# Kernel tuning notes

Hardware: AMD Instinct MI355X
Metric: run time of the kernel (lower is better)

Reference implementation:

```python
import jax, jax.numpy as jnp
import numpy as np

B, T, C, H = 2, 64, 384, 768
LR, MOM, DECAY = 0.01, 0.9, 0.001


def pscan(gates, tokens):
    """parallel_scan_log: x[t] = gates[t]*x[t-1] + tokens[t] along axis 1.
    gates [B,S], tokens [B,S,...]."""
    extra = tokens.ndim - gates.ndim
    g = gates.reshape(gates.shape + (1,) * extra)
    g = jnp.clip(g, 1e-7, 1.0 - 1e-7)
    lc = jnp.cumsum(jnp.log(g), axis=1)              # log cumulative gates
    return jnp.exp(lc) * jnp.cumsum(tokens * jnp.exp(-lc), axis=1)


def setup_inputs():
    key = jax.random.key(0)
    ks = jax.random.split(key, 12)
    s = 0.02
    W0 = jax.random.normal(ks[0], (H, C), jnp.float32) * s
    W1 = jax.random.normal(ks[1], (C, H), jnp.float32) * s
    return {
        "x": jax.random.normal(ks[2], (B, T, C), jnp.float32),
        "Wq": jax.random.normal(ks[3], (C, C), jnp.float32) * s, "bq": jnp.zeros((C,), jnp.float32),
        "Wk": jax.random.normal(ks[4], (C, C), jnp.float32) * s, "bk": jnp.zeros((C,), jnp.float32),
        "Wv": jax.random.normal(ks[5], (C, C), jnp.float32) * s, "bv": jnp.zeros((C,), jnp.float32),
        "Wo": jax.random.normal(ks[6], (C, C), jnp.float32) * s, "bo": jnp.zeros((C,), jnp.float32),
        "init_query": jax.random.normal(ks[7], (1, 1, C), jnp.float32) * s,
        "sW0": jnp.broadcast_to(W0, (B, H, C)) + 0.0,
        "sb0": jnp.zeros((B, H), jnp.float32),
        "sW1": jnp.broadcast_to(W1, (B, C, H)) + 0.0,
        "sb1": jnp.zeros((B, C), jnp.float32),
    }


def reference(x, Wq, bq, Wk, bk, Wv, bv, Wo, bo, init_query, sW0, sb0, sW1, sb1):
    dt = x.dtype
    # ---- retrieval (causal: uses init_query since no previous segment) ----
    q = jnp.broadcast_to(init_query, (B, 1, C)) @ Wq.T + bq          # [B,1,C]
    h_pre = jnp.einsum('bqc,bhc->bqh', q, sW0) + sb0[:, None]
    h = h_pre * jax.nn.sigmoid(h_pre)                                 # SiLU
    pred = jnp.einsum('bqh,bch->bqc', h, sW1) + sb1[:, None]
    out = pred @ Wo.T + bo                                            # [B,1,C]

    # ---- test-time memory update: per-token MSE gradients ----
    k = x @ Wk.T + bk                                                 # [B,T,C]
    v = x @ Wv.T + bv
    h1_pre = jnp.einsum('btc,bhc->bth', k, sW0) + sb0[:, None]
    sig = jax.nn.sigmoid(h1_pre)
    h1 = h1_pre * sig
    p = jnp.einsum('bth,bch->btc', h1, sW1) + sb1[:, None]
    dp = p - v                                                        # d(MSE)/d(pred)
    dW1 = jnp.einsum('btc,bth->btch', dp, h1)                         # [B,T,C,H]
    db1 = dp
    dh1 = jnp.einsum('btc,bch->bth', dp, sW1)
    dh1p = dh1 * (sig * (1 + h1_pre * (1 - sig)))                     # SiLU grad
    dW0 = jnp.einsum('bth,btc->bthc', dh1p, k)                        # [B,T,H,C]
    db0 = dh1p

    # ---- momentum scan + decayed weight scan ----
    def update(W, g):
        surprise = -LR * g                                            # [B,T,...]
        m = pscan(jnp.full((B, T), MOM, dt), (1.0 - MOM) * surprise)  # EMA of surprises
        toks = jnp.concatenate([W[:, None], m], axis=1)               # seed with current weight
        gts = jnp.concatenate([jnp.ones((B, 1), dt),
                               jnp.full((B, T), 1.0 - DECAY, dt)], axis=1)
        return pscan(gts, toks)[:, -1]                                # final weight after segment

    nW0 = update(sW0, dW0)
    nb0 = update(sb0, db0)
    nW1 = update(sW1, dW1)
    nb1 = update(sb1, db1)
    return out, nW0, nb0, nW1, nb1
```

## Files before the change

kernel.cpp:

```cpp
#include <hip/hip_runtime.h>
#include <hip/hip_bf16.h>
#include <cmath>

#define BB 2
#define TT 64
#define CC 384
#define HH 768

#define O_OUT 0
#define O_NW0 768
#define O_NB0 (768 + 589824)
#define O_NW1 (O_NB0 + 1536)
#define O_NB1 (O_NW1 + 589824)

struct Coefs { float ct[TT]; float dfac; };

typedef __attribute__((ext_vector_type(8))) short bf16x8;
typedef __attribute__((ext_vector_type(4))) float f32x4;

__device__ __forceinline__ float bf2f(unsigned short u) {
    union { unsigned int i; float f; } x; x.i = ((unsigned int)u) << 16; return x.f;
}
__device__ __forceinline__ unsigned short f2bf(float f) {
    union { float f; unsigned int i; } u; u.f = f;
    unsigned int x = u.i;
    unsigned int r = (x + 0x7fffu + ((x >> 16) & 1u)) >> 16;
    return (unsigned short)r;
}
__device__ __forceinline__ f32x4 mfma16(bf16x8 a, bf16x8 b, f32x4 c) {
    return __builtin_amdgcn_mfma_f32_16x16x32_bf16(a, b, c, 0, 0, 0);
}
__device__ __forceinline__ bf16x8 ldbf8(const unsigned short* p) {
    return *(const bf16x8*)p;
}

__global__ void k_conv(const float* __restrict__ x,  const float* __restrict__ Wq,
                       const float* __restrict__ Wk, const float* __restrict__ Wv,
                       const float* __restrict__ Wo, const float* __restrict__ sW0,
                       const float* __restrict__ sW1,
                       unsigned short* __restrict__ x_bf,  unsigned short* __restrict__ Wq_bf,
                       unsigned short* __restrict__ Wk_bf, unsigned short* __restrict__ Wv_bf,
                       unsigned short* __restrict__ Wo_bf, unsigned short* __restrict__ sW0_bf,
                       unsigned short* __restrict__ sW1_bf, unsigned short* __restrict__ sW1T_bf) {
    const int blk = blockIdx.x, j = threadIdx.x;
    if (blk < 1776) {
        int g = blk * 256 + j;
        const float* src; unsigned short* dst; int off;
        if      (g < 12288)  { src = x;   dst = x_bf;   off = g; }
        else if (g < 49152)  { src = Wq;  dst = Wq_bf;  off = g - 12288; }
        else if (g < 86016)  { src = Wk;  dst = Wk_bf;  off = g - 49152; }
        else if (g < 122880) { src = Wv;  dst = Wv_bf;  off = g - 86016; }
        else if (g < 159744) { src = Wo;  dst = Wo_bf;  off = g - 122880; }
        else if (g < 307200) { src = sW0; dst = sW0_bf; off = g - 159744; }
        else                 { src = sW1; dst = sW1_bf; off = g - 307200; }
        float4 v = ((const float4*)src)[off];
        ushort4 u;
        u.x = f2bf(v.x); u.y = f2bf(v.y); u.z = f2bf(v.z); u.w = f2bf(v.w);
        ((ushort4*)dst)[off] = u;
    } else {
        __shared__ float tile[32][33];
        const int r2 = blk - 1776;
        const int b = r2 / 288, rem = r2 % 288;
        const int c0 = (rem / 24) * 32, h0 = (rem % 24) * 32;
        const int row0 = j / 32, col = j % 32;
        #pragma unroll
        for (int r = 0; r < 4; ++r) {
            int row = row0 + r * 8;
            tile[row][col] = sW1[((size_t)(b * CC + c0 + row)) * HH + h0 + col];
        }
        __syncthreads();
        #pragma unroll
        for (int r = 0; r < 4; ++r) {
            int row = row0 + r * 8;
            sW1T_bf[((size_t)(b * HH + h0 + row)) * CC + c0 + col] = f2bf(tile[col][row]);
        }
    }
}

__global__ void k_qkv(const unsigned short* __restrict__ x_bf,
                      const unsigned short* __restrict__ Wk_bf, const float* __restrict__ bk,
                      const unsigned short* __restrict__ Wv_bf, const float* __restrict__ bv,
                      const unsigned short* __restrict__ Wq_bf, const float* __restrict__ bq,
                      const float* __restrict__ iq,
                      unsigned short* __restrict__ kb_bf, float* __restrict__ vb,
                      float* __restrict__ qb) {
    __shared__ float vecs[CC];
    __shared__ float part[16][17];
    const int blk = blockIdx.x, j = threadIdx.x;
    if (blk < 24) {
        const int wid = j >> 6, L = j & 63;
        const int w = blk * 4 + wid;
        const int mp = w % 4, np = w / 4;
        const int lrow = L & 15, kq = (L >> 4) * 8;
        const unsigned short* A0 = x_bf + (size_t)(mp * 32 + lrow) * CC;
        const unsigned short* A1 = A0 + 16 * CC;
        const int n0 = (2 * np) * 16 + lrow, n1 = n0 + 16;
        const unsigned short* B0 = (n0 < CC) ? (Wk_bf + (size_t)n0 * CC) : (Wv_bf + (size_t)(n0 - CC) * CC);
        const unsigned short* B1 = (n1 < CC) ? (Wk_bf + (size_t)n1 * CC) : (Wv_bf + (size_t)(n1 - CC) * CC);
        f32x4 acc00 = {0,0,0,0}, acc01 = {0,0,0,0}, acc10 = {0,0,0,0}, acc11 = {0,0,0,0};
        for (int s = 0; s < CC / 32; ++s) {
            int k = s * 32 + kq;
            bf16x8 a0 = ldbf8(A0 + k), a1 = ldbf8(A1 + k);
            bf16x8 b0 = ldbf8(B0 + k), b1 = ldbf8(B1 + k);
            acc00 = mfma16(a0, b0, acc00); acc01 = mfma16(a0, b1, acc01);
            acc10 = mfma16(a1, b0, acc10); acc11 = mfma16(a1, b1, acc11);
        }
        const int quad = L >> 4;
        #pragma unroll
        for (int mi = 0; mi < 2; ++mi) {
            #pragma unroll
            for (int ni = 0; ni < 2; ++ni) {
                f32x4 acc = mi == 0 ? (ni == 0 ? acc00 : acc01) : (ni == 0 ? acc10 : acc11);
                int n = (2 * np + ni) * 16 + lrow;
                #pragma unroll
                for (int r = 0; r < 4; ++r) {
                    int m = mp * 32 + mi * 16 + quad * 4 + r;
                    float v = acc[r];
                    if (n < CC) kb_bf[(size_t)m * CC + n] = f2bf(v + bk[n]);
                    else        vb[(size_t)m * CC + (n - CC)] = v + bv[n - CC];
                }
            }
        }
    } else {
        if (j < CC / 4) ((float4*)vecs)[j] = ((const float4*)iq)[j];
        __syncthreads();
        const int nt = blk - 24;
        const int nl = j & 15, ks = j >> 4;
        const int n = nt * 16 + nl;
        const unsigned short* wr = Wq_bf + (size_t)n * CC + ks * 24;
        float s = 0.f;
        for (int i = 0; i < 3; ++i) {
            bf16x8 wv8 = ldbf8(wr + i * 8);
            #pragma unroll
            for (int e = 0; e < 8; ++e)
                s += bf2f((unsigned short)wv8[e]) * vecs[ks * 24 + i * 8 + e];
        }
        part[ks][nl] = s;
        __syncthreads();
        if (j < 16) {
            float acc = bq[nt * 16 + j];
            #pragma unroll
            for (int kk = 0; kk < 16; ++kk) acc += part[kk][j];
            qb[nt * 16 + j] = acc;
        }
    }
}

__global__ void k_h1(const unsigned short* __restrict__ kb_bf, const float* __restrict__ qb,
                     const unsigned short* __restrict__ sW0_bf, const float* __restrict__ sb0,
                     unsigned short* __restrict__ h1_bf, float* __restrict__ dsil,
                     float* __restrict__ hret) {
    __shared__ float vecs[CC];
    __shared__ float part[16][17];
    const int blk = blockIdx.x, j = threadIdx.x;
    if (blk < 24) {
        const int b = blk / 12;
        const int wid = j >> 6, L = j & 63;
        const int w = (blk % 12) * 4 + wid;
        const int mp = w & 1, np = w >> 1;
        const int lrow = L & 15, kq = (L >> 4) * 8;
        const unsigned short* A0 = kb_bf + (size_t)(b * TT + mp * 32 + lrow) * CC;
        const unsigned short* A1 = A0 + 16 * CC;
        const int n0 = (2 * np) * 16 + lrow;
        const unsigned short* B0 = sW0_bf + (size_t)(b * HH + n0) * CC;
        const unsigned short* B1 = B0 + 16 * CC;
        f32x4 acc00 = {0,0,0,0}, acc01 = {0,0,0,0}, acc10 = {0,0,0,0}, acc11 = {0,0,0,0};
        for (int s = 0; s < CC / 32; ++s) {
            int k = s * 32 + kq;
            bf16x8 a0 = ldbf8(A0 + k), a1 = ldbf8(A1 + k);
            bf16x8 b0 = ldbf8(B0 + k), b1 = ldbf8(B1 + k);
            acc00 = mfma16(a0, b0, acc00); acc01 = mfma16(a0, b1, acc01);
            acc10 = mfma16(a1, b0, acc10); acc11 = mfma16(a1, b1, acc11);
        }
        const int quad = L >> 4;
        #pragma unroll
        for (int mi = 0; mi < 2; ++mi) {
            #pragma unroll
            for (int ni = 0; ni < 2; ++ni) {
                f32x4 acc = mi == 0 ? (ni == 0 ? acc00 : acc01) : (ni == 0 ? acc10 : acc11);
                int n = (2 * np + ni) * 16 + lrow;
                float bias = sb0[b * HH + n];
                #pragma unroll
                for (int r = 0; r < 4; ++r) {
                    int t = mp * 32 + mi * 16 + quad * 4 + r;
                    float pre = acc[r] + bias;
                    float sig = 1.f / (1.f + expf(-pre));
                    size_t idx = (size_t)(b * TT + t) * HH + n;
                    h1_bf[idx] = f2bf(pre * sig);
                    dsil[idx]  = sig * (1.f + pre * (1.f - sig));
                }
            }
        }
    } else {
        if (j < CC / 4) ((float4*)vecs)[j] = ((const float4*)qb)[j];
        __syncthreads();
        const int rb = blk - 24;
        const int b = rb / 48, nt = rb % 48;
        const int nl = j & 15, ks = j >> 4;
        const int n = nt * 16 + nl;
        const unsigned short* wr = sW0_bf + (size_t)(b * HH + n) * CC + ks * 24;
        float s = 0.f;
        for (int i = 0; i < 3; ++i) {
            bf16x8 wv8 = ldbf8(wr + i * 8);
            #pragma unroll
            for (int e = 0; e < 8; ++e)
                s += bf2f((unsigned short)wv8[e]) * vecs[ks * 24 + i * 8 + e];
        }
        part[ks][nl] = s;
        __syncthreads();
        if (j < 16) {
            int n2 = nt * 16 + j;
            float pre = sb0[b * HH + n2];
            #pragma unroll
            for (int kk = 0; kk < 16; ++kk) pre += part[kk][j];
            float sig = 1.f / (1.f + expf(-pre));
            hret[b * HH + n2] = pre * sig;
        }
    }
}

__global__ void k_p(const unsigned short* __restrict__ h1_bf, const float* __restrict__ hret,
                    const float* __restrict__ vb,
                    const unsigned short* __restrict__ sW1_bf, const float* __restrict__ sb1,
                    unsigned short* __restrict__ dp_bf, float* __restrict__ pred) {
    __shared__ float vecs[HH];
    __shared__ float part[16][17];
    const int blk = blockIdx.x, j = threadIdx.x;
    if (blk < 12) {
        const int b = blk / 6;
        const int wid = j >> 6, L = j & 63;
        const int w = (blk % 6) * 4 + wid;
        const int mp = w & 1, np = w >> 1;
        const int lrow = L & 15, kq = (L >> 4) * 8;
        const unsigned short* A0 = h1_bf + (size_t)(b * TT + mp * 32 + lrow) * HH;
        const unsigned short* A1 = A0 + 16 * HH;
        const int n0 = (2 * np) * 16 + lrow;
        const unsigned short* B0 = sW1_bf + (size_t)(b * CC + n0) * HH;
        const unsigned short* B1 = B0 + 16 * HH;
        f32x4 acc00 = {0,0,0,0}, acc01 = {0,0,0,0}, acc10 = {0,0,0,0}, acc11 = {0,0,0,0};
        for (int s = 0; s < HH / 32; ++s) {
            int k = s * 32 + kq;
            bf16x8 a0 = ldbf8(A0 + k), a1 = ldbf8(A1 + k);
            bf16x8 b0 = ldbf8(B0 + k), b1 = ldbf8(B1 + k);
            acc00 = mfma16(a0, b0, acc00); acc01 = mfma16(a0, b1, acc01);
            acc10 = mfma16(a1, b0, acc10); acc11 = mfma16(a1, b1, acc11);
        }
        const int quad = L >> 4;
        #pragma unroll
        for (int mi = 0; mi < 2; ++mi) {
            #pragma unroll
            for (int ni = 0; ni < 2; ++ni) {
                f32x4 acc = mi == 0 ? (ni == 0 ? acc00 : acc01) : (ni == 0 ? acc10 : acc11);
                int n = (2 * np + ni) * 16 + lrow;
                float bias = sb1[b * CC + n];
                #pragma unroll
                for (int r = 0; r < 4; ++r) {
                    int t = mp * 32 + mi * 16 + quad * 4 + r;
                    size_t idx = (size_t)(b * TT + t) * CC + n;
                    dp_bf[idx] = f2bf(acc[r] + bias - vb[idx]);
                }
            }
        }
    } else {
        const int rb = blk - 12;
        const int b = rb / 24, nt = rb % 24;
        if (j < HH / 4) ((float4*)vecs)[j] = ((const float4*)(hret + b * HH))[j];
        __syncthreads();
        const int nl = j & 15, ks = j >> 4;
        const int n = nt * 16 + nl;
        const unsigned short* wr = sW1_bf + (size_t)(b * CC + n) * HH + ks * 48;
        float s = 0.f;
        for (int i = 0; i < 6; ++i) {
            bf16x8 wv8 = ldbf8(wr + i * 8);
            #pragma unroll
            for (int e = 0; e < 8; ++e)
                s += bf2f((unsigned short)wv8[e]) * vecs[ks * 48 + i * 8 + e];
        }
        part[ks][nl] = s;
        __syncthreads();
        if (j < 16) {
            int n2 = nt * 16 + j;
            float acc = sb1[b * CC + n2];
            #pragma unroll
            for (int kk = 0; kk < 16; ++kk) acc += part[kk][j];
            pred[b * CC + n2] = acc;
        }
    }
}

__global__ void k_dh1(const unsigned short* __restrict__ dp_bf,
                      const unsigned short* __restrict__ sW1T_bf,
                      const float* __restrict__ dsil,
                      unsigned short* __restrict__ dh1p_bf) {
    const int blk = blockIdx.x, j = threadIdx.x;
    const int b = blk / 12;
    const int wid = j >> 6, L = j & 63;
    const int w = (blk % 12) * 4 + wid;
    const int mp = w & 1, np = w >> 1;
    const int lrow = L & 15, kq = (L >> 4) * 8;
    const unsigned short* A0 = dp_bf + (size_t)(b * TT + mp * 32 + lrow) * CC;
    const unsigned short* A1 = A0 + 16 * CC;
    const int n0 = (2 * np) * 16 + lrow;
    const unsigned short* B0 = sW1T_bf + (size_t)(b * HH + n0) * CC;
    const unsigned short* B1 = B0 + 16 * CC;
    f32x4 acc00 = {0,0,0,0}, acc01 = {0,0,0,0}, acc10 = {0,0,0,0}, acc11 = {0,0,0,0};
    for (int s = 0; s < CC / 32; ++s) {
        int k = s * 32 + kq;
        bf16x8 a0 = ldbf8(A0 + k), a1 = ldbf8(A1 + k);
        bf16x8 b0 = ldbf8(B0 + k), b1 = ldbf8(B1 + k);
        acc00 = mfma16(a0, b0, acc00); acc01 = mfma16(a0, b1, acc01);
        acc10 = mfma16(a1, b0, acc10); acc11 = mfma16(a1, b1, acc11);
    }
    const int quad = L >> 4;
    #pragma unroll
    for (int mi = 0; mi < 2; ++mi) {
        #pragma unroll
        for (int ni = 0; ni < 2; ++ni) {
            f32x4 acc = mi == 0 ? (ni == 0 ? acc00 : acc01) : (ni == 0 ? acc10 : acc11);
            int n = (2 * np + ni) * 16 + lrow;
            #pragma unroll
            for (int r = 0; r < 4; ++r) {
                int t = mp * 32 + mi * 16 + quad * 4 + r;
                size_t idx = (size_t)(b * TT + t) * HH + n;
                dh1p_bf[idx] = f2bf(acc[r] * dsil[idx]);
            }
        }
    }
}

__global__ void k_epi(const unsigned short* __restrict__ dp_bf,
                      const unsigned short* __restrict__ h1_bf,
                      const unsigned short* __restrict__ dh1p_bf,
                      const unsigned short* __restrict__ kb_bf,
                      const float* __restrict__ pred,
                      const float* __restrict__ sW0, const float* __restrict__ sb0,
                      const float* __restrict__ sW1, const float* __restrict__ sb1,
                      const unsigned short* __restrict__ Wo_bf, const float* __restrict__ bo,
                      float* __restrict__ out, Coefs cf) {
    __shared__ float a_t[TT][32];
    __shared__ float e_t[TT][64];
    __shared__ float vecs[CC];
    __shared__ float part[16][17];
    const int blk = blockIdx.x, j = threadIdx.x;

    if (blk < 288) {
        const int b = blk / 144, rem = blk % 144;
        const int c0 = (rem / 12) * 32, h0 = (rem % 12) * 64;
        for (int i = j; i < TT * 32; i += 256) {
            int t = i >> 5, c = i & 31;
            a_t[t][c] = cf.ct[t] * bf2f(dp_bf[((size_t)(b * TT + t)) * CC + c0 + c]);
        }
        for (int i = j; i < TT * 64; i += 256) {
            int t = i >> 6, h = i & 63;
            e_t[t][h] = bf2f(h1_bf[((size_t)(b * TT + t)) * HH + h0 + h]);
        }
        __syncthreads();
        const int ci = j & 31, hb = (j >> 5) * 8;
        float acc[8] = {0, 0, 0, 0, 0, 0, 0, 0};
        for (int t = 0; t < TT; ++t) {
            float av = a_t[t][ci];
            #pragma unroll
            for (int m = 0; m < 8; ++m) acc[m] += av * e_t[t][hb + m];
        }
        const size_t idx = ((size_t)b * CC + c0 + ci) * HH + h0 + hb;
        const float4* w4 = (const float4*)(sW1 + idx);
        float4 wa = w4[0], wb = w4[1];
        float4 o0, o1;
        o0.x = cf.dfac * wa.x - acc[0]; o0.y = cf.dfac * wa.y - acc[1];
        o0.z = cf.dfac * wa.z - acc[2]; o0.w = cf.dfac * wa.w - acc[3];
        o1.x = cf.dfac * wb.x - acc[4]; o1.y = cf.dfac * wb.y - acc[5];
        o1.z = cf.dfac * wb.z - acc[6]; o1.w = cf.dfac * wb.w - acc[7];
        *(float4*)(out + O_NW1 + idx) = o0;
        *(float4*)(out + O_NW1 + idx + 4) = o1;
    } else if (blk < 576) {
        const int bk2 = blk - 288;
        const int b = bk2 / 144, rem = bk2 % 144;
        const int h0 = (rem / 6) * 32, c0 = (rem % 6) * 64;
        for (int i = j; i < TT * 32; i += 256) {
            int t = i >> 5, h = i & 31;
            a_t[t][h] = cf.ct[t] * bf2f(dh1p_bf[((size_t)(b * TT + t)) * HH + h0 + h]);
        }
        for (int i = j; i < TT * 64; i += 256) {
            int t = i >> 6, c = i & 63;
            e_t[t][c] = bf2f(kb_bf[((size_t)(b * TT + t)) * CC + c0 + c]);
        }
        __syncthreads();
        const int hi = j & 31, cb = (j >> 5) * 8;
        float acc[8] = {0, 0, 0, 0, 0, 0, 0, 0};
        for (int t = 0; t < TT; ++t) {
            float av = a_t[t][hi];
            #pragma unroll
            for (int m = 0; m < 8; ++m) acc[m] += av * e_t[t][cb + m];
        }
        const size_t idx = ((size_t)b * HH + h0 + hi) * CC + c0 + cb;
        const float4* w4 = (const float4*)(sW0 + idx);
        float4 wa = w4[0], wb = w4[1];
        float4 o0, o1;
        o0.x = cf.dfac * wa.x - acc[0]; o0.y = cf.dfac * wa.y - acc[1];
        o0.z = cf.dfac * wa.z - acc[2]; o0.w = cf.dfac * wa.w - acc[3];
        o1.x = cf.dfac * wb.x - acc[4]; o1.y = cf.dfac * wb.y - acc[5];
        o1.z = cf.dfac * wb.z - acc[6]; o1.w = cf.dfac * wb.w - acc[7];
        *(float4*)(out + O_NW0 + idx) = o0;
        *(float4*)(out + O_NW0 + idx + 4) = o1;
    } else if (blk < 624) {
        const int rb = blk - 576;
        const int b = rb / 24, nt = rb % 24;
        if (j < CC / 4) ((float4*)vecs)[j] = ((const float4*)(pred + b * CC))[j];
        __syncthreads();
        const int nl = j & 15, ks = j >> 4;
        const int n = nt * 16 + nl;
        const unsigned short* wr = Wo_bf + (size_t)n * CC + ks * 24;
        float s = 0.f;
        for (int i = 0; i < 3; ++i) {
            bf16x8 wv8 = ldbf8(wr + i * 8);
            #pragma unroll
            for (int e = 0; e < 8; ++e)
                s += bf2f((unsigned short)wv8[e]) * vecs[ks * 24 + i * 8 + e];
        }
        part[ks][nl] = s;
        __syncthreads();
        if (j < 16) {
            int n2 = nt * 16 + j;
            float acc = bo[n2];
            #pragma unroll
            for (int kk = 0; kk < 16; ++kk) acc += part[kk][j];
            out[O_OUT + b * CC + n2] = acc;
        }
    } else {
        const int b = blk - 624;
        for (int c = j; c < CC; c += 256) {
            float acc = 0.f;
            for (int t = 0; t < TT; ++t)
                acc += cf.ct[t] * bf2f(dp_bf[((size_t)(b * TT + t)) * CC + c]);
            out[O_NB1 + b * CC + c] = cf.dfac * sb1[b * CC + c] - acc;
        }
        for (int h = j; h < HH; h += 256) {
            float acc = 0.f;
            for (int t = 0; t < TT; ++t)
                acc += cf.ct[t] * bf2f(dh1p_bf[((size_t)(b * TT + t)) * HH + h]);
            out[O_NB0 + b * HH + h] = cf.dfac * sb0[b * HH + h] - acc;
        }
    }
}

extern "C" void kernel_launch(void* const* d_in, const int* in_sizes, int n_in,
                              void* d_out, int out_size, void* d_ws, size_t ws_size,
                              hipStream_t stream) {
    const float* x   = (const float*)d_in[0];
    const float* Wq  = (const float*)d_in[1];
    const float* bq  = (const float*)d_in[2];
    const float* Wk  = (const float*)d_in[3];
    const float* bk  = (const float*)d_in[4];
    const float* Wv  = (const float*)d_in[5];
    const float* bv  = (const float*)d_in[6];
    const float* Wo  = (const float*)d_in[7];
    const float* bo  = (const float*)d_in[8];
    const float* iq  = (const float*)d_in[9];
    const float* sW0 = (const float*)d_in[10];
    const float* sb0 = (const float*)d_in[11];
    const float* sW1 = (const float*)d_in[12];
    const float* sb1 = (const float*)d_in[13];

    float* fw = (float*)d_ws;
    float* qb   = fw;
    float* hret = qb + 384;
    float* pred = hret + 1536;
    float* vb   = pred + 768;
    float* dsil = vb + 49152;
    unsigned short* us = (unsigned short*)(dsil + 98304);
    unsigned short* x_bf    = us;
    unsigned short* kb_bf   = x_bf + 49152;
    unsigned short* h1_bf   = kb_bf + 49152;
    unsigned short* dp_bf   = h1_bf + 98304;
    unsigned short* dh1p_bf = dp_bf + 49152;
    unsigned short* Wq_bf   = dh1p_bf + 98304;
    unsigned short* Wk_bf   = Wq_bf + 147456;
    unsigned short* Wv_bf   = Wk_bf + 147456;
    unsigned short* Wo_bf   = Wv_bf + 147456;
    unsigned short* sW0_bf  = Wo_bf + 147456;
    unsigned short* sW1_bf  = sW0_bf + 589824;
    unsigned short* sW1T_bf = sW1_bf + 589824;

    Coefs cf;
    const double mom = 0.9, decay = 1.0 - 0.001, lr = 0.01;
    for (int s = 0; s < TT; ++s) {
        double sum = 0.0;
        for (int t = s; t < TT; ++t) sum += pow(decay, (double)(TT - 1 - t)) * pow(mom, (double)(t - s));
        cf.ct[s] = (float)(lr * (1.0 - mom) * sum);
    }
    cf.dfac = (float)pow(decay, (double)TT);

    k_conv<<<dim3(1776 + 576), dim3(256), 0, stream>>>(x, Wq, Wk, Wv, Wo, sW0, sW1,
        x_bf, Wq_bf, Wk_bf, Wv_bf, Wo_bf, sW0_bf, sW1_bf, sW1T_bf);
    k_qkv<<<dim3(48), dim3(256), 0, stream>>>(x_bf, Wk_bf, bk, Wv_bf, bv, Wq_bf, bq, iq,
                                              kb_bf, vb, qb);
    k_h1 <<<dim3(120), dim3(256), 0, stream>>>(kb_bf, qb, sW0_bf, sb0, h1_bf, dsil, hret);
    k_p  <<<dim3(60), dim3(256), 0, stream>>>(h1_bf, hret, vb, sW1_bf, sb1, dp_bf, pred);
    k_dh1<<<dim3(24), dim3(256), 0, stream>>>(dp_bf, sW1T_bf, dsil, dh1p_bf);
    k_epi<<<dim3(626), dim3(256), 0, stream>>>(dp_bf, h1_bf, dh1p_bf, kb_bf, pred,
                                               sW0, sb0, sW1, sb1, Wo_bf, bo,
                                               (float*)d_out, cf);
}
```

Measured before the change: 144.6 us.

## Fuse six launches into one cooperative kernel with grid-wide syncs

Replaces the six separate kernel launches with one persistent cooperative kernel of 512 blocks whose stages are separated by grid.sync(). It also drops the bf16 conversions of Wq and Wo; the matrix-vector paths now read fp32 weights directly. The sW1 transpose pass writes both the plain and transposed bf16 copies from one shared tile. The aim is to remove per-launch overhead and gaps between launches, at the cost of grid barriers and many idle blocks in the small stages.

Measured after the change: 449.3 us. +210.6%, slower.

```diff
diff --git a/kernel.cpp b/kernel.cpp
--- a/kernel.cpp
+++ b/kernel.cpp
@@ -1,11 +1,15 @@
 #include <hip/hip_runtime.h>
 #include <hip/hip_bf16.h>
+#include <hip/hip_cooperative_groups.h>
 #include <cmath>
+
+namespace cg = cooperative_groups;
 
 #define BB 2
 #define TT 64
 #define CC 384
 #define HH 768
+#define GRID 512
 
 #define O_OUT 0
 #define O_NW0 768
@@ -18,6 +22,15 @@
 typedef __attribute__((ext_vector_type(8))) short bf16x8;
 typedef __attribute__((ext_vector_type(4))) float f32x4;
 
+struct Args {
+    const float *x, *Wq, *bq, *Wk, *bk, *Wv, *bv, *Wo, *bo, *iq, *sW0, *sb0, *sW1, *sb1;
+    unsigned short *x_bf, *Wk_bf, *Wv_bf, *sW0_bf, *sW1_bf, *sW1T_bf;
+    unsigned short *kb_bf, *h1_bf, *dp_bf, *dh1p_bf;
+    float *vb, *dsil, *qb, *hret, *pred;
+    float *out;
+    Coefs cf;
+};
+
 __device__ __forceinline__ float bf2f(unsigned short u) {
     union { unsigned int i; float f; } x; x.i = ((unsigned int)u) << 16; return x.f;
 }
@@ -34,69 +47,56 @@
     return *(const bf16x8*)p;
 }
 
-__global__ void k_conv(const float* __restrict__ x,  const float* __restrict__ Wq,
-                       const float* __restrict__ Wk, const float* __restrict__ Wv,
-                       const float* __restrict__ Wo, const float* __restrict__ sW0,
-                       const float* __restrict__ sW1,
-                       unsigned short* __restrict__ x_bf,  unsigned short* __restrict__ Wq_bf,
-                       unsigned short* __restrict__ Wk_bf, unsigned short* __restrict__ Wv_bf,
-                       unsigned short* __restrict__ Wo_bf, unsigned short* __restrict__ sW0_bf,
-                       unsigned short* __restrict__ sW1_bf, unsigned short* __restrict__ sW1T_bf) {
+__global__ void __launch_bounds__(256, 2) k_fused(Args A) {
+    __shared__ float smem[6144];
+    cg::grid_group grid = cg::this_grid();
     const int blk = blockIdx.x, j = threadIdx.x;
-    if (blk < 1776) {
-        int g = blk * 256 + j;
-        const float* src; unsigned short* dst; int off;
-        if      (g < 12288)  { src = x;   dst = x_bf;   off = g; }
-        else if (g < 49152)  { src = Wq;  dst = Wq_bf;  off = g - 12288; }
-        else if (g < 86016)  { src = Wk;  dst = Wk_bf;  off = g - 49152; }
-        else if (g < 122880) { src = Wv;  dst = Wv_bf;  off = g - 86016; }
-        else if (g < 159744) { src = Wo;  dst = Wo_bf;  off = g - 122880; }
-        else if (g < 307200) { src = sW0; dst = sW0_bf; off = g - 159744; }
-        else                 { src = sW1; dst = sW1_bf; off = g - 307200; }
-        float4 v = ((const float4*)src)[off];
-        ushort4 u;
-        u.x = f2bf(v.x); u.y = f2bf(v.y); u.z = f2bf(v.z); u.w = f2bf(v.w);
-        ((ushort4*)dst)[off] = u;
-    } else {
-        __shared__ float tile[32][33];
-        const int r2 = blk - 1776;
-        const int b = r2 / 288, rem = r2 % 288;
-        const int c0 = (rem / 24) * 32, h0 = (rem % 24) * 32;
-        const int row0 = j / 32, col = j % 32;
-        #pragma unroll
-        for (int r = 0; r < 4; ++r) {
-            int row = row0 + r * 8;
-            tile[row][col] = sW1[((size_t)(b * CC + c0 + row)) * HH + h0 + col];
-        }
-        __syncthreads();
-        #pragma unroll
-        for (int r = 0; r < 4; ++r) {
-            int row = row0 + r * 8;
-            sW1T_bf[((size_t)(b * HH + h0 + row)) * CC + c0 + col] = f2bf(tile[col][row]);
-        }
-    }
-}
-
-__global__ void k_qkv(const unsigned short* __restrict__ x_bf,
-                      const unsigned short* __restrict__ Wk_bf, const float* __restrict__ bk,
-                      const unsigned short* __restrict__ Wv_bf, const float* __restrict__ bv,
-                      const unsigned short* __restrict__ Wq_bf, const float* __restrict__ bq,
-                      const float* __restrict__ iq,
-                      unsigned short* __restrict__ kb_bf, float* __restrict__ vb,
-                      float* __restrict__ qb) {
-    __shared__ float vecs[CC];
-    __shared__ float part[16][17];
-    const int blk = blockIdx.x, j = threadIdx.x;
+    const Coefs& cf = A.cf;
+
+    {
+        int tid = blk * 256 + j;
+        for (int g = tid; g < 233472; g += GRID * 256) {
+            const float* src; unsigned short* dst; int off;
+            if      (g < 12288) { src = A.x;   dst = A.x_bf;   off = g; }
+            else if (g < 49152) { src = A.Wk;  dst = A.Wk_bf;  off = g - 12288; }
+            else if (g < 86016) { src = A.Wv;  dst = A.Wv_bf;  off = g - 49152; }
+            else                { src = A.sW0; dst = A.sW0_bf; off = g - 86016; }
+            float4 v = ((const float4*)src)[off];
+            ushort4 u;
+            u.x = f2bf(v.x); u.y = f2bf(v.y); u.z = f2bf(v.z); u.w = f2bf(v.w);
+            ((ushort4*)dst)[off] = u;
+        }
+        for (int u = blk; u < 576; u += GRID) {
+            const int b = u / 288, rem = u % 288;
+            const int c0 = (rem / 24) * 32, h0 = (rem % 24) * 32;
+            const int row0 = j >> 5, col = j & 31;
+            __syncthreads();
+            #pragma unroll
+            for (int r = 0; r < 4; ++r) {
+                int row = row0 + r * 8;
+                smem[row * 33 + col] = A.sW1[((size_t)(b * CC + c0 + row)) * HH + h0 + col];
+            }
+            __syncthreads();
+            #pragma unroll
+            for (int r = 0; r < 4; ++r) {
+                int row = row0 + r * 8;
+                A.sW1_bf [((size_t)(b * CC + c0 + row)) * HH + h0 + col] = f2bf(smem[row * 33 + col]);
+                A.sW1T_bf[((size_t)(b * HH + h0 + row)) * CC + c0 + col] = f2bf(smem[col * 33 + row]);
+            }
+        }
+    }
+    grid.sync();
+
     if (blk < 24) {
         const int wid = j >> 6, L = j & 63;
         const int w = blk * 4 + wid;
         const int mp = w % 4, np = w / 4;
         const int lrow = L & 15, kq = (L >> 4) * 8;
-        const unsigned short* A0 = x_bf + (size_t)(mp * 32 + lrow) * CC;
+        const unsigned short* A0 = A.x_bf + (size_t)(mp * 32 + lrow) * CC;
         const unsigned short* A1 = A0 + 16 * CC;
         const int n0 = (2 * np) * 16 + lrow, n1 = n0 + 16;
-        const unsigned short* B0 = (n0 < CC) ? (Wk_bf + (size_t)n0 * CC) : (Wv_bf + (size_t)(n0 - CC) * CC);
-        const unsigned short* B1 = (n1 < CC) ? (Wk_bf + (size_t)n1 * CC) : (Wv_bf + (size_t)(n1 - CC) * CC);
+        const unsigned short* B0 = (n0 < CC) ? (A.Wk_bf + (size_t)n0 * CC) : (A.Wv_bf + (size_t)(n0 - CC) * CC);
+        const unsigned short* B1 = (n1 < CC) ? (A.Wk_bf + (size_t)n1 * CC) : (A.Wv_bf + (size_t)(n1 - CC) * CC);
         f32x4 acc00 = {0,0,0,0}, acc01 = {0,0,0,0}, acc10 = {0,0,0,0}, acc11 = {0,0,0,0};
         for (int s = 0; s < CC / 32; ++s) {
             int k = s * 32 + kq;
@@ -116,53 +116,46 @@
                 for (int r = 0; r < 4; ++r) {
                     int m = mp * 32 + mi * 16 + quad * 4 + r;
                     float v = acc[r];
-                    if (n < CC) kb_bf[(size_t)m * CC + n] = f2bf(v + bk[n]);
-                    else        vb[(size_t)m * CC + (n - CC)] = v + bv[n - CC];
+                    if (n < CC) A.kb_bf[(size_t)m * CC + n] = f2bf(v + A.bk[n]);
+                    else        A.vb[(size_t)m * CC + (n - CC)] = v + A.bv[n - CC];
                 }
             }
         }
-    } else {
-        if (j < CC / 4) ((float4*)vecs)[j] = ((const float4*)iq)[j];
+    } else if (blk < 48) {
+        if (j < CC / 4) ((float4*)smem)[j] = ((const float4*)A.iq)[j];
         __syncthreads();
         const int nt = blk - 24;
         const int nl = j & 15, ks = j >> 4;
         const int n = nt * 16 + nl;
-        const unsigned short* wr = Wq_bf + (size_t)n * CC + ks * 24;
+        const float4* wr = (const float4*)(A.Wq + (size_t)n * CC + ks * 24);
         float s = 0.f;
-        for (int i = 0; i < 3; ++i) {
-            bf16x8 wv8 = ldbf8(wr + i * 8);
-            #pragma unroll
-            for (int e = 0; e < 8; ++e)
-                s += bf2f((unsigned short)wv8[e]) * vecs[ks * 24 + i * 8 + e];
-        }
-        part[ks][nl] = s;
+        #pragma unroll
+        for (int i = 0; i < 6; ++i) {
+            float4 a = wr[i];
+            const float* v = smem + ks * 24 + i * 4;
+            s += a.x * v[0] + a.y * v[1] + a.z * v[2] + a.w * v[3];
+        }
+        smem[1024 + ks * 17 + nl] = s;
         __syncthreads();
         if (j < 16) {
-            float acc = bq[nt * 16 + j];
-            #pragma unroll
-            for (int kk = 0; kk < 16; ++kk) acc += part[kk][j];
-            qb[nt * 16 + j] = acc;
-        }
-    }
-}
-
-__global__ void k_h1(const unsigned short* __restrict__ kb_bf, const float* __restrict__ qb,
-                     const unsigned short* __restrict__ sW0_bf, const float* __restrict__ sb0,
-                     unsigned short* __restrict__ h1_bf, float* __restrict__ dsil,
-                     float* __restrict__ hret) {
-    __shared__ float vecs[CC];
-    __shared__ float part[16][17];
-    const int blk = blockIdx.x, j = threadIdx.x;
+            float acc = A.bq[nt * 16 + j];
+            #pragma unroll
+            for (int kk = 0; kk < 16; ++kk) acc += smem[1024 + kk * 17 + j];
+            A.qb[nt * 16 + j] = acc;
+        }
+    }
+    grid.sync();
+
     if (blk < 24) {
         const int b = blk / 12;
         const int wid = j >> 6, L = j & 63;
         const int w = (blk % 12) * 4 + wid;
         const int mp = w & 1, np = w >> 1;
         const int lrow = L & 15, kq = (L >> 4) * 8;
-        const unsigned short* A0 = kb_bf + (size_t)(b * TT + mp * 32 + lrow) * CC;
+        const unsigned short* A0 = A.kb_bf + (size_t)(b * TT + mp * 32 + lrow) * CC;
         const unsigned short* A1 = A0 + 16 * CC;
         const int n0 = (2 * np) * 16 + lrow;
-        const unsigned short* B0 = sW0_bf + (size_t)(b * HH + n0) * CC;
+        const unsigned short* B0 = A.sW0_bf + (size_t)(b * HH + n0) * CC;
         const unsigned short* B1 = B0 + 16 * CC;
         f32x4 acc00 = {0,0,0,0}, acc01 = {0,0,0,0}, acc10 = {0,0,0,0}, acc11 = {0,0,0,0};
         for (int s = 0; s < CC / 32; ++s) {
@@ -179,63 +172,56 @@
             for (int ni = 0; ni < 2; ++ni) {
                 f32x4 acc = mi == 0 ? (ni == 0 ? acc00 : acc01) : (ni == 0 ? acc10 : acc11);
                 int n = (2 * np + ni) * 16 + lrow;
-                float bias = sb0[b * HH + n];
+                float bias = A.sb0[b * HH + n];
                 #pragma unroll
                 for (int r = 0; r < 4; ++r) {
                     int t = mp * 32 + mi * 16 + quad * 4 + r;
                     float pre = acc[r] + bias;
                     float sig = 1.f / (1.f + expf(-pre));
                     size_t idx = (size_t)(b * TT + t) * HH + n;
-                    h1_bf[idx] = f2bf(pre * sig);
-                    dsil[idx]  = sig * (1.f + pre * (1.f - sig));
+                    A.h1_bf[idx] = f2bf(pre * sig);
+                    A.dsil[idx]  = sig * (1.f + pre * (1.f - sig));
                 }
             }
         }
-    } else {
-        if (j < CC / 4) ((float4*)vecs)[j] = ((const float4*)qb)[j];
+    } else if (blk < 120) {
+        if (j < CC / 4) ((float4*)smem)[j] = ((const float4*)A.qb)[j];
         __syncthreads();
         const int rb = blk - 24;
         const int b = rb / 48, nt = rb % 48;
         const int nl = j & 15, ks = j >> 4;
         const int n = nt * 16 + nl;
-        const unsigned short* wr = sW0_bf + (size_t)(b * HH + n) * CC + ks * 24;
+        const float4* wr = (const float4*)(A.sW0 + (size_t)(b * HH + n) * CC + ks * 24);
         float s = 0.f;
-        for (int i = 0; i < 3; ++i) {
-            bf16x8 wv8 = ldbf8(wr + i * 8);
-            #pragma unroll
-            for (int e = 0; e < 8; ++e)
-                s += bf2f((unsigned short)wv8[e]) * vecs[ks * 24 + i * 8 + e];
-        }
-        part[ks][nl] = s;
+        #pragma unroll
+        for (int i = 0; i < 6; ++i) {
+            float4 a = wr[i];
+            const float* v = smem + ks * 24 + i * 4;
+            s += a.x * v[0] + a.y * v[1] + a.z * v[2] + a.w * v[3];
+        }
+        smem[1024 + ks * 17 + nl] = s;
         __syncthreads();
         if (j < 16) {
             int n2 = nt * 16 + j;
-            float pre = sb0[b * HH + n2];
-            #pragma unroll
-            for (int kk = 0; kk < 16; ++kk) pre += part[kk][j];
+            float pre = A.sb0[b * HH + n2];
+            #pragma unroll
+            for (int kk = 0; kk < 16; ++kk) pre += smem[1024 + kk * 17 + j];
             float sig = 1.f / (1.f + expf(-pre));
-            hret[b * HH + n2] = pre * sig;
-        }
-    }
-}
-
-__global__ void k_p(const unsigned short* __restrict__ h1_bf, const float* __restrict__ hret,
-                    const float* __restrict__ vb,
-                    const unsigned short* __restrict__ sW1_bf, const float* __restrict__ sb1,
-                    unsigned short* __restrict__ dp_bf, float* __restrict__ pred) {
-    __shared__ float vecs[HH];
-    __shared__ float part[16][17];
-    const int blk = blockIdx.x, j = threadIdx.x;
+            A.hret[b * HH + n2] = pre * sig;
+        }
+    }
+    grid.sync();
+
     if (blk < 12) {
         const int b = blk / 6;
         const int wid = j >> 6, L = j & 63;
         const int w = (blk % 6) * 4 + wid;
         const int mp = w & 1, np = w >> 1;
         const int lrow = L & 15, kq = (L >> 4) * 8;
-        const unsigned short* A0 = h1_bf + (size_t)(b * TT + mp * 32 + lrow) * HH;
+        const unsigned short* A0 = A.h1_bf + (size_t)(b * TT + mp * 32 + lrow) * HH;
         const unsigned short* A1 = A0 + 16 * HH;
         const int n0 = (2 * np) * 16 + lrow;
-        const unsigned short* B0 = sW1_bf + (size_t)(b * CC + n0) * HH;
+        const unsigned short* B0 = A.sW1_bf + (size_t)(b * CC + n0) * HH;
         const unsigned short* B1 = B0 + 16 * HH;
         f32x4 acc00 = {0,0,0,0}, acc01 = {0,0,0,0}, acc10 = {0,0,0,0}, acc11 = {0,0,0,0};
         for (int s = 0; s < HH / 32; ++s) {
@@ -252,193 +238,182 @@
             for (int ni = 0; ni < 2; ++ni) {
                 f32x4 acc = mi == 0 ? (ni == 0 ? acc00 : acc01) : (ni == 0 ? acc10 : acc11);
                 int n = (2 * np + ni) * 16 + lrow;
-                float bias = sb1[b * CC + n];
+                float bias = A.sb1[b * CC + n];
                 #pragma unroll
                 for (int r = 0; r < 4; ++r) {
                     int t = mp * 32 + mi * 16 + quad * 4 + r;
                     size_t idx = (size_t)(b * TT + t) * CC + n;
-                    dp_bf[idx] = f2bf(acc[r] + bias - vb[idx]);
+                    A.dp_bf[idx] = f2bf(acc[r] + bias - A.vb[idx]);
                 }
             }
         }
-    } else {
+    } else if (blk < 60) {
         const int rb = blk - 12;
         const int b = rb / 24, nt = rb % 24;
-        if (j < HH / 4) ((float4*)vecs)[j] = ((const float4*)(hret + b * HH))[j];
+        if (j < HH / 4) ((float4*)smem)[j] = ((const float4*)(A.hret + b * HH))[j];
         __syncthreads();
         const int nl = j & 15, ks = j >> 4;
         const int n = nt * 16 + nl;
-        const unsigned short* wr = sW1_bf + (size_t)(b * CC + n) * HH + ks * 48;
+        const float4* wr = (const float4*)(A.sW1 + (size_t)(b * CC + n) * HH + ks * 48);
         float s = 0.f;
-        for (int i = 0; i < 6; ++i) {
-            bf16x8 wv8 = ldbf8(wr + i * 8);
-            #pragma unroll
-            for (int e = 0; e < 8; ++e)
-                s += bf2f((unsigned short)wv8[e]) * vecs[ks * 48 + i * 8 + e];
-        }
-        part[ks][nl] = s;
+        #pragma unroll
+        for (int i = 0; i < 12; ++i) {
+            float4 a = wr[i];
+            const float* v = smem + ks * 48 + i * 4;
+            s += a.x * v[0] + a.y * v[1] + a.z * v[2] + a.w * v[3];
+        }
+        smem[1024 + ks * 17 + nl] = s;
         __syncthreads();
         if (j < 16) {
             int n2 = nt * 16 + j;
-            float acc = sb1[b * CC + n2];
-            #pragma unroll
-            for (int kk = 0; kk < 16; ++kk) acc += part[kk][j];
-            pred[b * CC + n2] = acc;
-        }
-    }
-}
-
-__global__ void k_dh1(const unsigned short* __restrict__ dp_bf,
-                      const unsigned short* __restrict__ sW1T_bf,
-                      const float* __restrict__ dsil,
-                      unsigned short* __restrict__ dh1p_bf) {
-    const int blk = blockIdx.x, j = threadIdx.x;
-    const int b = blk / 12;
-    const int wid = j >> 6, L = j & 63;
-    const int w = (blk % 12) * 4 + wid;
-    const int mp = w & 1, np = w >> 1;
-    const int lrow = L & 15, kq = (L >> 4) * 8;
-    const unsigned short* A0 = dp_bf + (size_t)(b * TT + mp * 32 + lrow) * CC;
-    const unsigned short* A1 = A0 + 16 * CC;
-    const int n0 = (2 * np) * 16 + lrow;
-    const unsigned short* B0 = sW1T_bf + (size_t)(b * HH + n0) * CC;
-    const unsigned short* B1 = B0 + 16 * CC;
-    f32x4 acc00 = {0,0,0,0}, acc01 = {0,0,0,0}, acc10 = {0,0,0,0}, acc11 = {0,0,0,0};
-    for (int s = 0; s < CC / 32; ++s) {
-        int k = s * 32 + kq;
-        bf16x8 a0 = ldbf8(A0 + k), a1 = ldbf8(A1 + k);
-        bf16x8 b0 = ldbf8(B0 + k), b1 = ldbf8(B1 + k);
-        acc00 = mfma16(a0, b0, acc00); acc01 = mfma16(a0, b1, acc01);
-        acc10 = mfma16(a1, b0, acc10); acc11 = mfma16(a1, b1, acc11);
-    }
-    const int quad = L >> 4;
-    #pragma unroll
-    for (int mi = 0; mi < 2; ++mi) {
-        #pragma unroll
-        for (int ni = 0; ni < 2; ++ni) {
-            f32x4 acc = mi == 0 ? (ni == 0 ? acc00 : acc01) : (ni == 0 ? acc10 : acc11);
-            int n = (2 * np + ni) * 16 + lrow;
-            #pragma unroll
-            for (int r = 0; r < 4; ++r) {
-                int t = mp * 32 + mi * 16 + quad * 4 + r;
-                size_t idx = (size_t)(b * TT + t) * HH + n;
-                dh1p_bf[idx] = f2bf(acc[r] * dsil[idx]);
-            }
-        }
-    }
-}
-
-__global__ void k_epi(const unsigned short* __restrict__ dp_bf,
-                      const unsigned short* __restrict__ h1_bf,
-                      const unsigned short* __restrict__ dh1p_bf,
-                      const unsigned short* __restrict__ kb_bf,
-                      const float* __restrict__ pred,
-                      const float* __restrict__ sW0, const float* __restrict__ sb0,
-                      const float* __restrict__ sW1, const float* __restrict__ sb1,
-                      const unsigned short* __restrict__ Wo_bf, const float* __restrict__ bo,
-                      float* __restrict__ out, Coefs cf) {
-    __shared__ float a_t[TT][32];
-    __shared__ float e_t[TT][64];
-    __shared__ float vecs[CC];
-    __shared__ float part[16][17];
-    const int blk = blockIdx.x, j = threadIdx.x;
-
-    if (blk < 288) {
-        const int b = blk / 144, rem = blk % 144;
-        const int c0 = (rem / 12) * 32, h0 = (rem % 12) * 64;
-        for (int i = j; i < TT * 32; i += 256) {
-            int t = i >> 5, c = i & 31;
-            a_t[t][c] = cf.ct[t] * bf2f(dp_bf[((size_t)(b * TT + t)) * CC + c0 + c]);
-        }
-        for (int i = j; i < TT * 64; i += 256) {
-            int t = i >> 6, h = i & 63;
-            e_t[t][h] = bf2f(h1_bf[((size_t)(b * TT + t)) * HH + h0 + h]);
-        }
-        __syncthreads();
-        const int ci = j & 31, hb = (j >> 5) * 8;
-        float acc[8] = {0, 0, 0, 0, 0, 0, 0, 0};
-        for (int t = 0; t < TT; ++t) {
-            float av = a_t[t][ci];
-            #pragma unroll
-            for (int m = 0; m < 8; ++m) acc[m] += av * e_t[t][hb + m];
-        }
-        const size_t idx = ((size_t)b * CC + c0 + ci) * HH + h0 + hb;
-        const float4* w4 = (const float4*)(sW1 + idx);
-        float4 wa = w4[0], wb = w4[1];
-        float4 o0, o1;
-        o0.x = cf.dfac * wa.x - acc[0]; o0.y = cf.dfac * wa.y - acc[1];
-        o0.z = cf.dfac * wa.z - acc[2]; o0.w = cf.dfac * wa.w - acc[3];
-        o1.x = cf.dfac * wb.x - acc[4]; o1.y = cf.dfac * wb.y - acc[5];
-        o1.z = cf.dfac * wb.z - acc[6]; o1.w = cf.dfac * wb.w - acc[7];
-        *(float4*)(out + O_NW1 + idx) = o0;
-        *(float4*)(out + O_NW1 + idx + 4) = o1;
-    } else if (blk < 576) {
-        const int bk2 = blk - 288;
-        const int b = bk2 / 144, rem = bk2 % 144;
-        const int h0 = (rem / 6) * 32, c0 = (rem % 6) * 64;
-        for (int i = j; i < TT * 32; i += 256) {
-            int t = i >> 5, h = i & 31;
-            a_t[t][h] = cf.ct[t] * bf2f(dh1p_bf[((size_t)(b * TT + t)) * HH + h0 + h]);
-        }
-        for (int i = j; i < TT * 64; i += 256) {
-            int t = i >> 6, c = i & 63;
-            e_t[t][c] = bf2f(kb_bf[((size_t)(b * TT + t)) * CC + c0 + c]);
-        }
-        __syncthreads();
-        const int hi = j & 31, cb = (j >> 5) * 8;
-        float acc[8] = {0, 0, 0, 0, 0, 0, 0, 0};
-        for (int t = 0; t < TT; ++t) {
-            float av = a_t[t][hi];
-            #pragma unroll
-            for (int m = 0; m < 8; ++m) acc[m] += av * e_t[t][cb + m];
-        }
-        const size_t idx = ((size_t)b * HH + h0 + hi) * CC + c0 + cb;
-        const float4* w4 = (const float4*)(sW0 + idx);
-        float4 wa = w4[0], wb = w4[1];
-        float4 o0, o1;
-        o0.x = cf.dfac * wa.x - acc[0]; o0.y = cf.dfac * wa.y - acc[1];
-        o0.z = cf.dfac * wa.z - acc[2]; o0.w = cf.dfac * wa.w - acc[3];
-        o1.x = cf.dfac * wb.x - acc[4]; o1.y = cf.dfac * wb.y - acc[5];
-        o1.z = cf.dfac * wb.z - acc[6]; o1.w = cf.dfac * wb.w - acc[7];
-        *(float4*)(out + O_NW0 + idx) = o0;
-        *(float4*)(out + O_NW0 + idx + 4) = o1;
-    } else if (blk < 624) {
-        const int rb = blk - 576;
-        const int b = rb / 24, nt = rb % 24;
-        if (j < CC / 4) ((float4*)vecs)[j] = ((const float4*)(pred + b * CC))[j];
-        __syncthreads();
-        const int nl = j & 15, ks = j >> 4;
-        const int n = nt * 16 + nl;
-        const unsigned short* wr = Wo_bf + (size_t)n * CC + ks * 24;
-        float s = 0.f;
-        for (int i = 0; i < 3; ++i) {
-            bf16x8 wv8 = ldbf8(wr + i * 8);
-            #pragma unroll
-            for (int e = 0; e < 8; ++e)
-                s += bf2f((unsigned short)wv8[e]) * vecs[ks * 24 + i * 8 + e];
-        }
-        part[ks][nl] = s;
-        __syncthreads();
-        if (j < 16) {
-            int n2 = nt * 16 + j;
-            float acc = bo[n2];
-            #pragma unroll
-            for (int kk = 0; kk < 16; ++kk) acc += part[kk][j];
-            out[O_OUT + b * CC + n2] = acc;
-        }
-    } else {
-        const int b = blk - 624;
-        for (int c = j; c < CC; c += 256) {
-            float acc = 0.f;
-            for (int t = 0; t < TT; ++t)
-                acc += cf.ct[t] * bf2f(dp_bf[((size_t)(b * TT + t)) * CC + c]);
-            out[O_NB1 + b * CC + c] = cf.dfac * sb1[b * CC + c] - acc;
-        }
-        for (int h = j; h < HH; h += 256) {
-            float acc = 0.f;
-            for (int t = 0; t < TT; ++t)
-                acc += cf.ct[t] * bf2f(dh1p_bf[((size_t)(b * TT + t)) * HH + h]);
-            out[O_NB0 + b * HH + h] = cf.dfac * sb0[b * HH + h] - acc;
+            float acc = A.sb1[b * CC + n2];
+            #pragma unroll
+            for (int kk = 0; kk < 16; ++kk) acc += smem[1024 + kk * 17 + j];
+            A.pred[b * CC + n2] = acc;
+        }
+    }
+    grid.sync();
+
+    if (blk < 24) {
+        const int b = blk / 12;
+        const int wid = j >> 6, L = j & 63;
+        const int w = (blk % 12) * 4 + wid;
+        const int mp = w & 1, np = w >> 1;
+        const int lrow = L & 15, kq = (L >> 4) * 8;
+        const unsigned short* A0 = A.dp_bf + (size_t)(b * TT + mp * 32 + lrow) * CC;
+        const unsigned short* A1 = A0 + 16 * CC;
+        const int n0 = (2 * np) * 16 + lrow;
+        const unsigned short* B0 = A.sW1T_bf + (size_t)(b * HH + n0) * CC;
+        const unsigned short* B1 = B0 + 16 * CC;
+        f32x4 acc00 = {0,0,0,0}, acc01 = {0,0,0,0}, acc10 = {0,0,0,0}, acc11 = {0,0,0,0};
+        for (int s = 0; s < CC / 32; ++s) {
+            int k = s * 32 + kq;
+            bf16x8 a0 = ldbf8(A0 + k), a1 = ldbf8(A1 + k);
+            bf16x8 b0 = ldbf8(B0 + k), b1 = ldbf8(B1 + k);
+            acc00 = mfma16(a0, b0, acc00); acc01 = mfma16(a0, b1, acc01);
+            acc10 = mfma16(a1, b0, acc10); acc11 = mfma16(a1, b1, acc11);
+        }
+        const int quad = L >> 4;
+        #pragma unroll
+        for (int mi = 0; mi < 2; ++mi) {
+            #pragma unroll
+            for (int ni = 0; ni < 2; ++ni) {
+                f32x4 acc = mi == 0 ? (ni == 0 ? acc00 : acc01) : (ni == 0 ? acc10 : acc11);
+                int n = (2 * np + ni) * 16 + lrow;
+                #pragma unroll
+                for (int r = 0; r < 4; ++r) {
+                    int t = mp * 32 + mi * 16 + quad * 4 + r;
+                    size_t idx = (size_t)(b * TT + t) * HH + n;
+                    A.dh1p_bf[idx] = f2bf(acc[r] * A.dsil[idx]);
+                }
+            }
+        }
+    }
+    grid.sync();
+
+    for (int u = blk; u < 626; u += GRID) {
+        __syncthreads();
+        if (u < 288) {
+            float* a_t = smem;
+            float* e_t = smem + 2048;
+            const int b = u / 144, rem = u % 144;
+            const int c0 = (rem / 12) * 32, h0 = (rem % 12) * 64;
+            for (int i = j; i < TT * 32; i += 256) {
+                int t = i >> 5, c = i & 31;
+                a_t[t * 32 + c] = cf.ct[t] * bf2f(A.dp_bf[((size_t)(b * TT + t)) * CC + c0 + c]);
+            }
+            for (int i = j; i < TT * 64; i += 256) {
+                int t = i >> 6, h = i & 63;
+                e_t[t * 64 + h] = bf2f(A.h1_bf[((size_t)(b * TT + t)) * HH + h0 + h]);
+            }
+            __syncthreads();
+            const int ci = j & 31, hb = (j >> 5) * 8;
+            float acc[8] = {0, 0, 0, 0, 0, 0, 0, 0};
+            for (int t = 0; t < TT; ++t) {
+                float av = a_t[t * 32 + ci];
+                #pragma unroll
+                for (int m = 0; m < 8; ++m) acc[m] += av * e_t[t * 64 + hb + m];
+            }
+            const size_t idx = ((size_t)b * CC + c0 + ci) * HH + h0 + hb;
+            const float4* w4 = (const float4*)(A.sW1 + idx);
+            float4 wa = w4[0], wb = w4[1];
+            float4 o0, o1;
+            o0.x = cf.dfac * wa.x - acc[0]; o0.y = cf.dfac * wa.y - acc[1];
+            o0.z = cf.dfac * wa.z - acc[2]; o0.w = cf.dfac * wa.w - acc[3];
+            o1.x = cf.dfac * wb.x - acc[4]; o1.y = cf.dfac * wb.y - acc[5];
+            o1.z = cf.dfac * wb.z - acc[6]; o1.w = cf.dfac * wb.w - acc[7];
+            *(float4*)(A.out + O_NW1 + idx) = o0;
+            *(float4*)(A.out + O_NW1 + idx + 4) = o1;
+        } else if (u < 576) {
+            float* a_t = smem;
+            float* e_t = smem + 2048;
+            const int u2 = u - 288;
+            const int b = u2 / 144, rem = u2 % 144;
+            const int h0 = (rem / 6) * 32, c0 = (rem % 6) * 64;
+            for (int i = j; i < TT * 32; i += 256) {
+                int t = i >> 5, h = i & 31;
+                a_t[t * 32 + h] = cf.ct[t] * bf2f(A.dh1p_bf[((size_t)(b * TT + t)) * HH + h0 + h]);
+            }
+            for (int i = j; i < TT * 64; i += 256) {
+                int t = i >> 6, c = i & 63;
+                e_t[t * 64 + c] = bf2f(A.kb_bf[((size_t)(b * TT + t)) * CC + c0 + c]);
+            }
+            __syncthreads();
+            const int hi = j & 31, cb = (j >> 5) * 8;
+            float acc[8] = {0, 0, 0, 0, 0, 0, 0, 0};
+            for (int t = 0; t < TT; ++t) {
+                float av = a_t[t * 32 + hi];
+                #pragma unroll
+                for (int m = 0; m < 8; ++m) acc[m] += av * e_t[t * 64 + cb + m];
+            }
+            const size_t idx = ((size_t)b * HH + h0 + hi) * CC + c0 + cb;
+            const float4* w4 = (const float4*)(A.sW0 + idx);
+            float4 wa = w4[0], wb = w4[1];
+            float4 o0, o1;
+            o0.x = cf.dfac * wa.x - acc[0]; o0.y = cf.dfac * wa.y - acc[1];
+            o0.z = cf.dfac * wa.z - acc[2]; o0.w = cf.dfac * wa.w - acc[3];
+            o1.x = cf.dfac * wb.x - acc[4]; o1.y = cf.dfac * wb.y - acc[5];
+            o1.z = cf.dfac * wb.z - acc[6]; o1.w = cf.dfac * wb.w - acc[7];
+            *(float4*)(A.out + O_NW0 + idx) = o0;
+            *(float4*)(A.out + O_NW0 + idx + 4) = o1;
+        } else if (u < 624) {
+            const int rb = u - 576;
+            const int b = rb / 24, nt = rb % 24;
+            if (j < CC / 4) ((float4*)smem)[j] = ((const float4*)(A.pred + b * CC))[j];
+            __syncthreads();
+            const int nl = j & 15, ks = j >> 4;
+            const int n = nt * 16 + nl;
+            const float4* wr = (const float4*)(A.Wo + (size_t)n * CC + ks * 24);
+            float s = 0.f;
+            #pragma unroll
+            for (int i = 0; i < 6; ++i) {
+                float4 a = wr[i];
+                const float* v = smem + ks * 24 + i * 4;
+                s += a.x * v[0] + a.y * v[1] + a.z * v[2] + a.w * v[3];
+            }
+            smem[1024 + ks * 17 + nl] = s;
+            __syncthreads();
+            if (j < 16) {
+                int n2 = nt * 16 + j;
+                float acc = A.bo[n2];
+                #pragma unroll
+                for (int kk = 0; kk < 16; ++kk) acc += smem[1024 + kk * 17 + j];
+                A.out[O_OUT + b * CC + n2] = acc;
+            }
+        } else {
+            const int b = u - 624;
+            for (int c = j; c < CC; c += 256) {
+                float acc = 0.f;
+                for (int t = 0; t < TT; ++t)
+                    acc += cf.ct[t] * bf2f(A.dp_bf[((size_t)(b * TT + t)) * CC + c]);
+                A.out[O_NB1 + b * CC + c] = cf.dfac * A.sb1[b * CC + c] - acc;
+            }
+            for (int h = j; h < HH; h += 256) {
+                float acc = 0.f;
+                for (int t = 0; t < TT; ++t)
+                    acc += cf.ct[t] * bf2f(A.dh1p_bf[((size_t)(b * TT + t)) * HH + h]);
+                A.out[O_NB0 + b * HH + h] = cf.dfac * A.sb0[b * HH + h] - acc;
+            }
         }
     }
 }
@@ -446,58 +421,49 @@
 extern "C" void kernel_launch(void* const* d_in, const int* in_sizes, int n_in,
                               void* d_out, int out_size, void* d_ws, size_t ws_size,
                               hipStream_t stream) {
-    const float* x   = (const float*)d_in[0];
-    const float* Wq  = (const float*)d_in[1];
-    const float* bq  = (const float*)d_in[2];
-    const float* Wk  = (const float*)d_in[3];
-    const float* bk  = (const float*)d_in[4];
-    const float* Wv  = (const float*)d_in[5];
-    const float* bv  = (const float*)d_in[6];
-    const float* Wo  = (const float*)d_in[7];
-    const float* bo  = (const float*)d_in[8];
-    const float* iq  = (const float*)d_in[9];
-    const float* sW0 = (const float*)d_in[10];
-    const float* sb0 = (const float*)d_in[11];
-    const float* sW1 = (const float*)d_in[12];
-    const float* sb1 = (const float*)d_in[13];
+    Args A;
+    A.x   = (const float*)d_in[0];
+    A.Wq  = (const float*)d_in[1];
+    A.bq  = (const float*)d_in[2];
+    A.Wk  = (const float*)d_in[3];
+    A.bk  = (const float*)d_in[4];
+    A.Wv  = (const float*)d_in[5];
+    A.bv  = (const float*)d_in[6];
+    A.Wo  = (const float*)d_in[7];
+    A.bo  = (const float*)d_in[8];
+    A.iq  = (const float*)d_in[9];
+    A.sW0 = (const float*)d_in[10];
+    A.sb0 = (const float*)d_in[11];
+    A.sW1 = (const float*)d_in[12];
+    A.sb1 = (const float*)d_in[13];
+    A.out = (float*)d_out;
 
     float* fw = (float*)d_ws;
-    float* qb   = fw;
-    float* hret = qb + 384;
-    float* pred = hret + 1536;
-    float* vb   = pred + 768;
-    float* dsil = vb + 49152;
-    unsigned short* us = (unsigned short*)(dsil + 98304);
-    unsigned short* x_bf    = us;
-    unsigned short* kb_bf   = x_bf + 49152;
-    unsigned short* h1_bf   = kb_bf + 49152;
-    unsigned short* dp_bf   = h1_bf + 98304;
-    unsigned short* dh1p_bf = dp_bf + 49152;
-    unsigned short* Wq_bf   = dh1p_bf + 98304;
-    unsigned short* Wk_bf   = Wq_bf + 147456;
-    unsigned short* Wv_bf   = Wk_bf + 147456;
-    unsigned short* Wo_bf   = Wv_bf + 147456;
-    unsigned short* sW0_bf  = Wo_bf + 147456;
-    unsigned short* sW1_bf  = sW0_bf + 589824;
-    unsigned short* sW1T_bf = sW1_bf + 589824;
-
-    Coefs cf;
+    A.qb   = fw;
+    A.hret = A.qb + 384;
+    A.pred = A.hret + 1536;
+    A.vb   = A.pred + 768;
+    A.dsil = A.vb + 49152;
+    unsigned short* us = (unsigned short*)(A.dsil + 98304);
+    A.x_bf    = us;
+    A.kb_bf   = A.x_bf + 49152;
+    A.h1_bf   = A.kb_bf + 49152;
+    A.dp_bf   = A.h1_bf + 98304;
+    A.dh1p_bf = A.dp_bf + 49152;
+    A.Wk_bf   = A.dh1p_bf + 98304;
+    A.Wv_bf   = A.Wk_bf + 147456;
+    A.sW0_bf  = A.Wv_bf + 147456;
+    A.sW1_bf  = A.sW0_bf + 589824;
+    A.sW1T_bf = A.sW1_bf + 589824;
+
     const double mom = 0.9, decay = 1.0 - 0.001, lr = 0.01;
     for (int s = 0; s < TT; ++s) {
         double sum = 0.0;
         for (int t = s; t < TT; ++t) sum += pow(decay, (double)(TT - 1 - t)) * pow(mom, (double)(t - s));
-        cf.ct[s] = (float)(lr * (1.0 - mom) * sum);
-    }
-    cf.dfac = (float)pow(decay, (double)TT);
-
-    k_conv<<<dim3(1776 + 576), dim3(256), 0, stream>>>(x, Wq, Wk, Wv, Wo, sW0, sW1,
-        x_bf, Wq_bf, Wk_bf, Wv_bf, Wo_bf, sW0_bf, sW1_bf, sW1T_bf);
-    k_qkv<<<dim3(48), dim3(256), 0, stream>>>(x_bf, Wk_bf, bk, Wv_bf, bv, Wq_bf, bq, iq,
-                                              kb_bf, vb, qb);
-    k_h1 <<<dim3(120), dim3(256), 0, stream>>>(kb_bf, qb, sW0_bf, sb0, h1_bf, dsil, hret);
-    k_p  <<<dim3(60), dim3(256), 0, stream>>>(h1_bf, hret, vb, sW1_bf, sb1, dp_bf, pred);
-    k_dh1<<<dim3(24), dim3(256), 0, stream>>>(dp_bf, sW1T_bf, dsil, dh1p_bf);
-    k_epi<<<dim3(626), dim3(256), 0, stream>>>(dp_bf, h1_bf, dh1p_bf, kb_bf, pred,
-                                               sW0, sb0, sW1, sb1, Wo_bf, bo,
-                                               (float*)d_out, cf);
-}
+        A.cf.ct[s] = (float)(lr * (1.0 - mom) * sum);
+    }
+    A.cf.dfac = (float)pow(decay, (double)TT);
+
+    void* kargs[] = { (void*)&A };
+    hipLaunchCooperativeKernel((const void*)k_fused, dim3(GRID), dim3(256), kargs, 0, stream);
+}
```
